# Optimization experiments

Measured on AMD Instinct MI355X. Metric: run time of the kernel, lower is better.

Reference implementation:

```python
import jax, jax.numpy as jnp
import numpy as np

N = 20000      # nodes
E = 400000     # edges
D = 256        # input_dim == hidden_dim
L = 4          # num_layers
EIN = 32       # edgenet_input_dim // 2
EH = 128       # edge parser hidden
NC = 2         # num_classes
JK = L * D     # 1024
BN_EPS = 1e-5


def setup_inputs() -> dict:
    key = jax.random.key(0)
    ks = jax.random.split(key, 16)
    s = 0.05
    inp = {
        "features": jax.random.normal(ks[0], (N, D), jnp.float32),
        "edge_index": jax.random.randint(ks[1], (2, E), 0, N, dtype=jnp.int64),
        "edgenet_input": jax.random.normal(ks[2], (E, 2 * EIN), jnp.float32),
        # ChebConv weights: [layer, k, in, out] (all layers 256->256, K=3, no bias)
        "cheb_w": jax.random.normal(ks[3], (L, 3, D, D), jnp.float32) * s,
        # EdgeEncoder (PAE-style) parser: Linear(32,128)+ReLU+BN+Linear(128,128)
        "en_w1": jax.random.normal(ks[4], (EIN, EH), jnp.float32) * s,
        "en_b1": jnp.zeros((EH,), jnp.float32),
        "en_g1": jnp.ones((EH,), jnp.float32),
        "en_be1": jnp.zeros((EH,), jnp.float32),
        "en_w2": jax.random.normal(ks[5], (EH, EH), jnp.float32) * s,
        "en_b2": jnp.zeros((EH,), jnp.float32),
        # cls head: Linear(1024,256)+ReLU+BN(256)+Linear(256,2)
        "cls_w1": jax.random.normal(ks[6], (JK, 256), jnp.float32) * s,
        "cls_b1": jnp.zeros((256,), jnp.float32),
        "cls_g": jnp.ones((256,), jnp.float32),
        "cls_b": jnp.zeros((256,), jnp.float32),
        "cls_w2": jax.random.normal(ks[7], (256, NC), jnp.float32) * s,
        "cls_b2": jnp.zeros((NC,), jnp.float32),
    }
    return inp


def _bn_eval(x, g, b):
    # eval-mode BatchNorm1d with fresh running stats (mean=0, var=1)
    return x * (g / jnp.sqrt(1.0 + BN_EPS)) + b


def reference(features, edge_index, edgenet_input, cheb_w,
              en_w1, en_b1, en_g1, en_be1, en_w2, en_b2,
              cls_w1, cls_b1, cls_g, cls_b, cls_w2, cls_b2):
    row, col = edge_index[0], edge_index[1]

    # ---- EdgeEncoder (PAE): shared parser on both halves + cosine sim ----
    def parser(x):
        h = jnp.maximum(x @ en_w1 + en_b1, 0.0)
        h = _bn_eval(h, en_g1, en_be1)
        return h @ en_w2 + en_b2

    half = edgenet_input.shape[1] // 2
    h1 = parser(edgenet_input[:, :half])
    h2 = parser(edgenet_input[:, half:])
    n1 = jnp.maximum(jnp.linalg.norm(h1, axis=1), 1e-8)
    n2 = jnp.maximum(jnp.linalg.norm(h2, axis=1), 1e-8)
    cos = jnp.sum(h1 * h2, axis=1) / (n1 * n2)
    edge_weight = (cos + 1.0) * 0.5  # [E]

    # ---- ChebConv sym normalization (lambda_max=2): L_hat = -D^-1/2 A D^-1/2 ----
    deg = jax.ops.segment_sum(edge_weight, row, num_segments=N)
    dis = jnp.where(deg > 0, jax.lax.rsqrt(jnp.maximum(deg, 1e-30)), 0.0)
    norm = -dis[row] * edge_weight * dis[col]  # [E]

    def prop(x):  # out[col] += norm * x[row]
        return jax.ops.segment_sum(x[row] * norm[:, None], col, num_segments=N)

    # ---- stacked ChebConv (K=3, no bias) + ReLU + JK concat ----
    x = features
    jk = None
    for i in range(L):
        W = cheb_w[i]
        Tx0 = x
        Tx1 = prop(Tx0)
        Tx2 = 2.0 * prop(Tx1) - Tx0
        h = jnp.maximum(Tx0 @ W[0] + Tx1 @ W[1] + Tx2 @ W[2], 0.0)
        jk = h if i == 0 else jnp.concatenate([jk, h], axis=1)
        x = h

    # ---- cls head ----
    z = jnp.maximum(jk @ cls_w1 + cls_b1, 0.0)
    z = _bn_eval(z, cls_g, cls_b)
    logit = z @ cls_w2 + cls_b2
    return (logit, edge_weight)
```

## Files before the change

kernel.cpp:

```cpp
#include <hip/hip_runtime.h>
#include <hip/hip_bf16.h>

#define NN 20000
#define EE 400000
#define RSBN 0.9999950000374997f

typedef __attribute__((ext_vector_type(8))) short short8;
typedef __attribute__((ext_vector_type(8))) unsigned short ushort8;
typedef __attribute__((ext_vector_type(4))) float floatx4;

__device__ __forceinline__ short f2bf(float f) {
  union { float f; unsigned u; } v; v.f = f;
  unsigned r = v.u + 0x7fffu + ((v.u >> 16) & 1u);
  return (short)(r >> 16);
}
__device__ __forceinline__ unsigned f2bf2(float x, float y) {
  union { __hip_bfloat162 h; unsigned u; } v;
  v.h = __float22bfloat162_rn(make_float2(x, y));
  return v.u;
}
__device__ __forceinline__ float bf2f(unsigned short u) {
  union { unsigned u; float f; } v; v.u = ((unsigned)u) << 16;
  return v.f;
}
__device__ __forceinline__ void gl_lds16(const void* g, void* l) {
  __builtin_amdgcn_global_load_lds(
      (const __attribute__((address_space(1))) unsigned*)g,
      (__attribute__((address_space(3))) unsigned*)l, 16, 0, 0);
}

__global__ __launch_bounds__(256) void ewconv_kernel(
    const float* __restrict__ w1, const float* __restrict__ w2,
    const float* __restrict__ g1, const float* __restrict__ be1,
    const float* __restrict__ b1, const float* __restrict__ b2,
    unsigned short* __restrict__ ewf)
{
  int tid = threadIdx.x;
#pragma unroll
  for (int i = 0; i < 16; i++) {
    int idx = i * 256 + tid;
    int k = idx >> 7, n = idx & 127;
    int pos = ((n >> 4) * 64 + (k >> 3) * 16 + (n & 15)) * 8 + (k & 7);
    ewf[pos] = f2bf(w1[idx]);
  }
#pragma unroll
  for (int i = 0; i < 64; i++) {
    int idx = i * 256 + tid;
    int k = idx >> 7, n = idx & 127;
    int pos = (((k >> 5) * 8 + (n >> 4)) * 64 + ((k >> 3) & 3) * 16 + (n & 15)) * 8 + (k & 7);
    ewf[4096 + pos] = f2bf(w2[idx] * g1[k] * RSBN);
  }
  float* fb = (float*)(ewf + 20480);
  if (tid < 128) {
    fb[tid] = b1[tid];
    float acc = b2[tid];
    for (int k = 0; k < 128; k++) acc += be1[k] * w2[k * 128 + tid] * g1[k] * RSBN;
    fb[128 + tid] = acc;
  }
}

#define ASP 136
__global__ __launch_bounds__(512, 4) void edge_kernel(
    const float* __restrict__ xin, const int* __restrict__ eidx,
    const unsigned short* __restrict__ ewf,
    float* __restrict__ ew_out,
    float* __restrict__ deg, int* __restrict__ cnt)
{
  __shared__ short wbuf[20992];
  __shared__ short as_s[128 * ASP];

  int tid = threadIdx.x;
  int lane = tid & 63;
  int wv = tid >> 6;
  int l15 = lane & 15;
  int quad = lane >> 4;

#pragma unroll
  for (int i = 0; i < 5; i++)
    gl_lds16(ewf + (i * 512 + tid) * 8, &wbuf[(i * 512 + tid) * 8]);
  if (tid < 64)
    gl_lds16(ewf + (2560 + tid) * 8, &wbuf[(2560 + tid) * 8]);

  const short* w1f = wbuf;
  const short* w2f = wbuf + 4096;

  int rowbase = blockIdx.x * 128 + wv * 16;

  short8 af;
  {
    const float* xp = xin + (size_t)(rowbase + l15) * 32 + quad * 8;
    float4 v0 = *(const float4*)xp;
    float4 v1 = *(const float4*)(xp + 4);
    union { short8 s; unsigned u[4]; } a;
    a.u[0] = f2bf2(v0.x, v0.y); a.u[1] = f2bf2(v0.z, v0.w);
    a.u[2] = f2bf2(v1.x, v1.y); a.u[3] = f2bf2(v1.z, v1.w);
    af = a.s;
  }

  __syncthreads();

  const float* fb = (const float*)(wbuf + 20480);
  float b1j[8], b2j[8];
#pragma unroll
  for (int c = 0; c < 8; c++) {
    b1j[c] = fb[c * 16 + l15];
    b2j[c] = fb[128 + c * 16 + l15];
  }

  floatx4 acc[8];
#pragma unroll
  for (int c = 0; c < 8; c++) {
    floatx4 z = {b1j[c], b1j[c], b1j[c], b1j[c]};
    acc[c] = __builtin_amdgcn_mfma_f32_16x16x32_bf16(
        af, *(const short8*)&w1f[(c * 64 + lane) * 8], z, 0, 0, 0);
  }

#pragma unroll
  for (int c = 0; c < 8; c++)
#pragma unroll
    for (int r = 0; r < 4; r += 2) {
      unsigned pk = f2bf2(fmaxf(acc[c][r], 0.f), fmaxf(acc[c][r + 1], 0.f));
      int base = (wv * 16 + quad * 4 + r) * ASP + c * 16 + l15;
      as_s[base] = (short)(pk & 0xffff);
      as_s[base + ASP] = (short)(pk >> 16);
    }

  floatx4 acc2[8];
#pragma unroll
  for (int c = 0; c < 8; c++) acc2[c] = (floatx4){b2j[c], b2j[c], b2j[c], b2j[c]};
#pragma unroll
  for (int s = 0; s < 4; s++) {
    short8 a2 = *(const short8*)&as_s[(wv * 16 + l15) * ASP + s * 32 + quad * 8];
#pragma unroll
    for (int c = 0; c < 8; c++) {
      short8 bf = *(const short8*)&w2f[((s * 8 + c) * 64 + lane) * 8];
      acc2[c] = __builtin_amdgcn_mfma_f32_16x16x32_bf16(a2, bf, acc2[c], 0, 0, 0);
    }
  }

  float p[2], qq[2], rr[2];
#pragma unroll
  for (int i = 0; i < 2; i++) { p[i] = 0.f; qq[i] = 0.f; rr[i] = 0.f; }
#pragma unroll
  for (int c = 0; c < 8; c++)
#pragma unroll
    for (int i = 0; i < 2; i++) {
      float hx = acc2[c][2 * i];
      float hy = acc2[c][2 * i + 1];
      p[i]  += hx * hy;
      qq[i] += hx * hx;
      rr[i] += hy * hy;
    }
#pragma unroll
  for (int m = 1; m < 16; m <<= 1)
#pragma unroll
    for (int i = 0; i < 2; i++) {
      p[i]  += __shfl_xor(p[i], m, 64);
      qq[i] += __shfl_xor(qq[i], m, 64);
      rr[i] += __shfl_xor(rr[i], m, 64);
    }
  if (l15 == 0) {
#pragma unroll
    for (int i = 0; i < 2; i++) {
      int row = rowbase + quad * 4 + 2 * i;
      int e = row >> 1;
      float n1 = fmaxf(sqrtf(qq[i]), 1e-8f);
      float n2 = fmaxf(sqrtf(rr[i]), 1e-8f);
      float w = (p[i] / (n1 * n2) + 1.f) * 0.5f;
      ew_out[e] = w;
      atomicAdd(deg + eidx[e], w);
      atomicAdd(cnt + eidx[EE + e], 1);
    }
  }
}

__global__ __launch_bounds__(256) void fconv_kernel(const float* __restrict__ src,
                                                    unsigned short* __restrict__ dst) {
  size_t i = ((size_t)blockIdx.x * 256 + threadIdx.x) * 8;
  float4 a = *(const float4*)(src + i);
  float4 b = *(const float4*)(src + i + 4);
  union { ushort8 s; unsigned u[4]; } o;
  o.u[0] = f2bf2(a.x, a.y); o.u[1] = f2bf2(a.z, a.w);
  o.u[2] = f2bf2(b.x, b.y); o.u[3] = f2bf2(b.z, b.w);
  *(ushort8*)(dst + i) = o.s;
}

__global__ __launch_bounds__(256) void wconv_kernel(
    const float* __restrict__ cheb_w, const float* __restrict__ cls_w1,
    unsigned short* __restrict__ wtc, unsigned short* __restrict__ clsT)
{
  __shared__ unsigned short tile[64][80];
  int z = blockIdx.z;
  const float* src; unsigned short* dst; int ldk;
  if (z < 12) {
    int l = z / 3, c = z % 3;
    src = cheb_w + (size_t)z * 65536;
    dst = wtc + (size_t)l * 196608 + c * 256;
    ldk = 768;
  } else {
    int c = z - 12;
    src = cls_w1 + (size_t)c * 65536;
    dst = clsT + c * 256;
    ldk = 1024;
  }
  int t = threadIdx.x;
  int k0 = blockIdx.x * 64, n0 = blockIdx.y * 64;
#pragma unroll
  for (int pass = 0; pass < 4; pass++) {
    int kk = pass * 16 + (t >> 4);
    int nl = (t & 15) * 4;
    float4 v = *(const float4*)(src + (size_t)(k0 + kk) * 256 + n0 + nl);
    tile[nl + 0][kk] = f2bf(v.x);
    tile[nl + 1][kk] = f2bf(v.y);
    tile[nl + 2][kk] = f2bf(v.z);
    tile[nl + 3][kk] = f2bf(v.w);
  }
  __syncthreads();
  int nl = t >> 2, kc = (t & 3) * 16;
  ushort8 v0 = *(const ushort8*)&tile[nl][kc];
  ushort8 v1 = *(const ushort8*)&tile[nl][kc + 8];
  unsigned short* dp = dst + (size_t)(n0 + nl) * ldk + k0 + kc;
  *(ushort8*)dp = v0;
  *(ushort8*)(dp + 8) = v1;
}

__global__ void dis_kernel(const float* __restrict__ deg, float* __restrict__ dis) {
  int i = blockIdx.x * 256 + threadIdx.x;
  if (i < NN) {
    float d = deg[i];
    dis[i] = d > 0.f ? 1.f / sqrtf(fmaxf(d, 1e-30f)) : 0.f;
  }
}

__global__ __launch_bounds__(1024) void scan_kernel(const int* __restrict__ cnt, int* __restrict__ ptr) {
  __shared__ int sums[1024];
  int tid = threadIdx.x;
  const int n = NN;
  const int chunk = (n + 1023) / 1024;
  int base = tid * chunk;
  int s = 0;
  for (int i = 0; i < chunk; i++) {
    int idx = base + i;
    if (idx < n) s += (cnt[idx] + 3) & ~3;
  }
  sums[tid] = s;
  __syncthreads();
  for (int off = 1; off < 1024; off <<= 1) {
    int v = (tid >= off) ? sums[tid - off] : 0;
    __syncthreads();
    sums[tid] += v;
    __syncthreads();
  }
  int run = (tid == 0) ? 0 : sums[tid - 1];
  for (int i = 0; i < chunk; i++) {
    int idx = base + i;
    if (idx < n) { ptr[idx] = run; run += (cnt[idx] + 3) & ~3; }
  }
  if (tid == 1023) ptr[n] = run;
}

__global__ void fill_kernel(const int* __restrict__ eidx, const float* __restrict__ ew,
                            const float* __restrict__ dis, const int* __restrict__ ptr,
                            int* __restrict__ fill, int* __restrict__ cidx, float* __restrict__ cval) {
  int e = blockIdx.x * 256 + threadIdx.x;
  if (e < EE) {
    int r = eidx[e], c = eidx[EE + e];
    float nv = -dis[r] * ew[e] * dis[c];
    int pos = ptr[c] + atomicAdd(&fill[c], 1);
    cidx[pos] = r;
    cval[pos] = nv;
  }
}

__global__ __launch_bounds__(256) void prop_kernel(
    const unsigned short* __restrict__ x, int ldx,
    const int* __restrict__ cidx, const float* __restrict__ cval,
    const int* __restrict__ ptr,
    unsigned short* __restrict__ y, int ldy,
    float alpha, const unsigned short* __restrict__ sub, int ldsub)
{
  int sliceid = blockIdx.x & 7;
  int colslice = sliceid >> 1;
  int chunk = (blockIdx.x >> 3) * 2 + (sliceid & 1);
  int c = chunk * 32 + (threadIdx.x >> 3);
  if (c >= NN) return;
  int d = colslice * 64 + (threadIdx.x & 7) * 8;
  int p0 = ptr[c], p1 = ptr[c + 1];
  float a[8] = {0.f, 0.f, 0.f, 0.f, 0.f, 0.f, 0.f, 0.f};
  if (p0 < p1) {
    int4 r4 = *(const int4*)(cidx + p0);
    float4 w4 = *(const float4*)(cval + p0);
    ushort8 v0 = *(const ushort8*)(x + (size_t)r4.x * ldx + d);
    ushort8 v1 = *(const ushort8*)(x + (size_t)r4.y * ldx + d);
    ushort8 v2 = *(const ushort8*)(x + (size_t)r4.z * ldx + d);
    ushort8 v3 = *(const ushort8*)(x + (size_t)r4.w * ldx + d);
    for (int p = p0 + 4; p < p1; p += 4) {
      int4 r4n = *(const int4*)(cidx + p);
      float4 w4n = *(const float4*)(cval + p);
      ushort8 n0 = *(const ushort8*)(x + (size_t)r4n.x * ldx + d);
      ushort8 n1 = *(const ushort8*)(x + (size_t)r4n.y * ldx + d);
      ushort8 n2 = *(const ushort8*)(x + (size_t)r4n.z * ldx + d);
      ushort8 n3 = *(const ushort8*)(x + (size_t)r4n.w * ldx + d);
#pragma unroll
      for (int j = 0; j < 8; j++)
        a[j] += w4.x * bf2f(v0[j]) + w4.y * bf2f(v1[j]) + w4.z * bf2f(v2[j]) + w4.w * bf2f(v3[j]);
      w4 = w4n; v0 = n0; v1 = n1; v2 = n2; v3 = n3;
    }
#pragma unroll
    for (int j = 0; j < 8; j++)
      a[j] += w4.x * bf2f(v0[j]) + w4.y * bf2f(v1[j]) + w4.z * bf2f(v2[j]) + w4.w * bf2f(v3[j]);
  }
  union { ushort8 s; unsigned u[4]; } o;
  if (sub) {
    ushort8 sv = *(const ushort8*)(sub + (size_t)c * ldsub + d);
#pragma unroll
    for (int j = 0; j < 8; j += 2)
      o.u[j >> 1] = f2bf2(alpha * a[j] - bf2f(sv[j]), alpha * a[j + 1] - bf2f(sv[j + 1]));
  } else {
#pragma unroll
    for (int j = 0; j < 8; j += 2)
      o.u[j >> 1] = f2bf2(a[j], a[j + 1]);
  }
  *(ushort8*)(y + (size_t)c * ldy + d) = o.s;
}

__global__ __launch_bounds__(256, 4) void mgemm_kernel(
    const unsigned short* A0, const unsigned short* A1,
    const unsigned short* A2, const unsigned short* A3,
    int l0, int l1, int l2, int l3, int nchunks,
    const unsigned short* __restrict__ BT, int ldbt,
    unsigned short* __restrict__ Cb, float* __restrict__ Cf, int ldc, int M,
    const float* __restrict__ bias, const float* __restrict__ bng,
    const float* __restrict__ bnb)
{
  __shared__ short As[4 * 64 * 8];
  __shared__ short Bs[4 * 128 * 8];
  int tid = threadIdx.x;
  int lane = tid & 63;
  int wv = tid >> 6;
  int l15 = lane & 15, quad = lane >> 4;
  int wr = wv >> 1, wc = wv & 1;
  int m0 = blockIdx.x * 64, n0 = blockIdx.y * 128;

  const unsigned short* Ap[4] = {A0, A1, A2, A3};
  int Al[4] = {l0, l1, l2, l3};

  int arow = tid & 63, ac = tid >> 6;
  int brow = tid & 127, bc = tid >> 7;

  floatx4 acc[2][4];
#pragma unroll
  for (int mi = 0; mi < 2; mi++)
#pragma unroll
    for (int nj = 0; nj < 4; nj++) acc[mi][nj] = (floatx4){0.f, 0.f, 0.f, 0.f};

  for (int c = 0; c < nchunks; c++) {
    const unsigned short* Abase = Ap[c] + (size_t)(m0 + arow) * Al[c] + ac * 8;
    const unsigned short* Bbase = BT + (size_t)(n0 + brow) * ldbt + c * 256 + bc * 8;
#pragma unroll 1
    for (int kb = 0; kb < 256; kb += 32) {
      __syncthreads();
      gl_lds16(Abase + kb, &As[tid * 8]);
      gl_lds16(Bbase + kb, &Bs[tid * 8]);
      gl_lds16(Bbase + 16 + kb, &Bs[(tid + 256) * 8]);
      __syncthreads();
      short8 af[2], bfv[4];
#pragma unroll
      for (int mi = 0; mi < 2; mi++)
        af[mi] = *(const short8*)&As[(quad * 64 + wr * 32 + mi * 16 + l15) * 8];
#pragma unroll
      for (int nj = 0; nj < 4; nj++)
        bfv[nj] = *(const short8*)&Bs[(quad * 128 + wc * 64 + nj * 16 + l15) * 8];
#pragma unroll
      for (int nj = 0; nj < 4; nj++)
#pragma unroll
        for (int mi = 0; mi < 2; mi++)
          acc[mi][nj] = __builtin_amdgcn_mfma_f32_16x16x32_bf16(af[mi], bfv[nj], acc[mi][nj], 0, 0, 0);
    }
  }

  if (Cb) {
#pragma unroll
    for (int mi = 0; mi < 2; mi++)
#pragma unroll
      for (int r = 0; r < 4; r++) {
        int row = m0 + wr * 32 + mi * 16 + quad * 4 + r;
        if (row < M) {
#pragma unroll
          for (int nj = 0; nj < 4; nj++) {
            int col = n0 + wc * 64 + nj * 16 + l15;
            Cb[(size_t)row * ldc + col] = (unsigned short)f2bf(fmaxf(acc[mi][nj][r], 0.f));
          }
        }
      }
  } else {
    float bs[4], g[4], bb[4];
#pragma unroll
    for (int nj = 0; nj < 4; nj++) {
      int col = n0 + wc * 64 + nj * 16 + l15;
      bs[nj] = bias[col]; g[nj] = bng[col] * RSBN; bb[nj] = bnb[col];
    }
#pragma unroll
    for (int mi = 0; mi < 2; mi++)
#pragma unroll
      for (int r = 0; r < 4; r++) {
        int row = m0 + wr * 32 + mi * 16 + quad * 4 + r;
        if (row < M) {
#pragma unroll
          for (int nj = 0; nj < 4; nj++) {
            int col = n0 + wc * 64 + nj * 16 + l15;
            float v = fmaxf(acc[mi][nj][r] + bs[nj], 0.f) * g[nj] + bb[nj];
            Cf[(size_t)row * ldc + col] = v;
          }
        }
      }
  }
}

__global__ __launch_bounds__(256) void logit_kernel(
    const float* __restrict__ z, const float* __restrict__ w2,
    const float* __restrict__ b2, float* __restrict__ out)
{
  int node = blockIdx.x * 4 + (threadIdx.x >> 6);
  if (node >= NN) return;
  int lane = threadIdx.x & 63;
  int k = lane * 4;
  float4 zv = *(const float4*)(z + (size_t)node * 256 + k);
  float4 wa = *(const float4*)(w2 + k * 2);
  float4 wb = *(const float4*)(w2 + k * 2 + 4);
  float a0 = zv.x * wa.x + zv.y * wa.z + zv.z * wb.x + zv.w * wb.z;
  float a1 = zv.x * wa.y + zv.y * wa.w + zv.z * wb.y + zv.w * wb.w;
#pragma unroll
  for (int m = 32; m >= 1; m >>= 1) {
    a0 += __shfl_xor(a0, m, 64);
    a1 += __shfl_xor(a1, m, 64);
  }
  if (lane == 0) {
    out[(size_t)node * 2]     = a0 + b2[0];
    out[(size_t)node * 2 + 1] = a1 + b2[1];
  }
}

extern "C" void kernel_launch(void* const* d_in, const int* in_sizes, int n_in,
                              void* d_out, int out_size, void* d_ws, size_t ws_size,
                              hipStream_t stream) {
  const float* features = (const float*)d_in[0];
  const int*   eidx     = (const int*)d_in[1];
  const float* xin      = (const float*)d_in[2];
  const float* cheb_w   = (const float*)d_in[3];
  const float* en_w1    = (const float*)d_in[4];
  const float* en_b1    = (const float*)d_in[5];
  const float* en_g1    = (const float*)d_in[6];
  const float* en_be1   = (const float*)d_in[7];
  const float* en_w2    = (const float*)d_in[8];
  const float* en_b2    = (const float*)d_in[9];
  const float* cls_w1   = (const float*)d_in[10];
  const float* cls_b1   = (const float*)d_in[11];
  const float* cls_g    = (const float*)d_in[12];
  const float* cls_b    = (const float*)d_in[13];
  const float* cls_w2   = (const float*)d_in[14];
  const float* cls_b2   = (const float*)d_in[15];
  float* out = (float*)d_out;

  char* ws = (char*)d_ws;
  size_t off = 0;
  auto alloc = [&](size_t bytes) -> void* {
    void* p = ws + off;
    off += (bytes + 255) & ~(size_t)255;
    return p;
  };
  const int CSRN = EE + 4 * NN;
  float* deg  = (float*)alloc((size_t)NN * 4);
  int*   cnt  = (int*)  alloc((size_t)NN * 4);
  int*   fil  = (int*)  alloc((size_t)NN * 4);
  float* cval = (float*)alloc((size_t)CSRN * 4);
  int*   cidx = (int*)  alloc((size_t)CSRN * 4);
  size_t zero_len = off;
  float* dis  = (float*)alloc((size_t)NN * 4);
  int*   ptr  = (int*)  alloc((size_t)(NN + 1) * 4);
  unsigned short* featb = (unsigned short*)alloc((size_t)NN * 256 * 2);
  unsigned short* Tx1   = (unsigned short*)alloc((size_t)NN * 256 * 2);
  unsigned short* Tx2   = (unsigned short*)alloc((size_t)NN * 256 * 2);
  unsigned short* jk    = (unsigned short*)alloc((size_t)NN * 1024 * 2);
  float* zbuf = (float*)alloc((size_t)NN * 256 * 4);
  unsigned short* wtc   = (unsigned short*)alloc((size_t)4 * 196608 * 2);
  unsigned short* clsT  = (unsigned short*)alloc((size_t)256 * 1024 * 2);
  unsigned short* ewf   = (unsigned short*)alloc((size_t)20992 * 2);
  alloc(262144);

  float* ew = out + (size_t)NN * 2;

  hipMemsetAsync(deg, 0, zero_len, stream);

  ewconv_kernel<<<1, 256, 0, stream>>>(en_w1, en_w2, en_g1, en_be1, en_b1, en_b2, ewf);
  edge_kernel<<<6250, 512, 0, stream>>>(xin, eidx, ewf, ew, deg, cnt);
  fconv_kernel<<<2500, 256, 0, stream>>>(features, featb);
  wconv_kernel<<<dim3(4, 4, 16), 256, 0, stream>>>(cheb_w, cls_w1, wtc, clsT);
  dis_kernel<<<(NN + 255) / 256, 256, 0, stream>>>(deg, dis);
  scan_kernel<<<1, 1024, 0, stream>>>(cnt, ptr);
  fill_kernel<<<(EE + 255) / 256, 256, 0, stream>>>(eidx, ew, dis, ptr, fil, cidx, cval);

  dim3 ggrid(313, 2);
  for (int i = 0; i < 4; i++) {
    const unsigned short* x = (i == 0) ? featb : (jk + (size_t)(i - 1) * 256);
    int ldx = (i == 0) ? 256 : 1024;
    prop_kernel<<<2504, 256, 0, stream>>>(x, ldx, cidx, cval, ptr, Tx1, 256, 1.f, nullptr, 0);
    prop_kernel<<<2504, 256, 0, stream>>>(Tx1, 256, cidx, cval, ptr, Tx2, 256, 2.f, x, ldx);
    mgemm_kernel<<<ggrid, 256, 0, stream>>>(x, Tx1, Tx2, nullptr, ldx, 256, 256, 0, 3,
                                            wtc + (size_t)i * 196608, 768,
                                            jk + (size_t)i * 256, nullptr, 1024, NN,
                                            nullptr, nullptr, nullptr);
  }

  mgemm_kernel<<<ggrid, 256, 0, stream>>>(jk, jk + 256, jk + 512, jk + 768,
                                          1024, 1024, 1024, 1024, 4, clsT, 1024,
                                          nullptr, zbuf, 256, NN,
                                          cls_b1, cls_g, cls_b);
  logit_kernel<<<NN / 4, 256, 0, stream>>>(zbuf, cls_w2, cls_b2, out);
}
```

Baseline: 646.8 us.

## Keep edge MLP hidden activations in registers and fold dis into fill

The edge encoder now computes the first layer transposed, so the ReLU output already sits in the B-operand layout of a 16x16x16 bf16 MFMA for the second layer. This removes the shared-memory staging buffer and its round trip. The W2 prepack layout and the cosine reduction shuffles are changed to match, and launch bounds rise to 6 blocks per CU. Separately, the dis kernel is removed and fill_kernel computes rsqrt(deg) inline, trading one launch for redundant per-edge rsqrt work.

```diff
diff --git a/kernel.cpp b/kernel.cpp
--- a/kernel.cpp
+++ b/kernel.cpp
@@ -7,6 +7,7 @@
 
 typedef __attribute__((ext_vector_type(8))) short short8;
 typedef __attribute__((ext_vector_type(8))) unsigned short ushort8;
+typedef __attribute__((ext_vector_type(4))) short bf4;
 typedef __attribute__((ext_vector_type(4))) float floatx4;
 
 __device__ __forceinline__ short f2bf(float f) {
@@ -27,6 +28,17 @@
   __builtin_amdgcn_global_load_lds(
       (const __attribute__((address_space(1))) unsigned*)g,
       (__attribute__((address_space(3))) unsigned*)l, 16, 0, 0);
+}
+
+__device__ __forceinline__ floatx4 mfma16(bf4 a, bf4 b, floatx4 c) {
+#if __has_builtin(__builtin_amdgcn_mfma_f32_16x16x16bf16_1k)
+  return __builtin_amdgcn_mfma_f32_16x16x16bf16_1k(a, b, c, 0, 0, 0);
+#else
+  floatx4 d;
+  asm volatile("v_mfma_f32_16x16x16_bf16 %0, %1, %2, %3"
+               : "=&v"(d) : "v"(a), "v"(b), "v"(c));
+  return d;
+#endif
 }
 
 __global__ __launch_bounds__(256) void ewconv_kernel(
@@ -47,7 +59,9 @@
   for (int i = 0; i < 64; i++) {
     int idx = i * 256 + tid;
     int k = idx >> 7, n = idx & 127;
-    int pos = (((k >> 5) * 8 + (n >> 4)) * 64 + ((k >> 3) & 3) * 16 + (n & 15)) * 8 + (k & 7);
+    int u = k >> 4, q = (k >> 2) & 3, j = k & 3;
+    int t = n >> 4, l = n & 15;
+    int pos = (((u * 8 + t) * 4 + q) * 16 + l) * 4 + j;
     ewf[4096 + pos] = f2bf(w2[idx] * g1[k] * RSBN);
   }
   float* fb = (float*)(ewf + 20480);
@@ -59,15 +73,13 @@
   }
 }
 
-#define ASP 136
-__global__ __launch_bounds__(512, 4) void edge_kernel(
+__global__ __launch_bounds__(512, 6) void edge_kernel(
     const float* __restrict__ xin, const int* __restrict__ eidx,
     const unsigned short* __restrict__ ewf,
     float* __restrict__ ew_out,
     float* __restrict__ deg, int* __restrict__ cnt)
 {
   __shared__ short wbuf[20992];
-  __shared__ short as_s[128 * ASP];
 
   int tid = threadIdx.x;
   int lane = tid & 63;
@@ -100,77 +112,60 @@
   __syncthreads();
 
   const float* fb = (const float*)(wbuf + 20480);
-  float b1j[8], b2j[8];
-#pragma unroll
-  for (int c = 0; c < 8; c++) {
-    b1j[c] = fb[c * 16 + l15];
-    b2j[c] = fb[128 + c * 16 + l15];
-  }
-
-  floatx4 acc[8];
-#pragma unroll
-  for (int c = 0; c < 8; c++) {
-    floatx4 z = {b1j[c], b1j[c], b1j[c], b1j[c]};
-    acc[c] = __builtin_amdgcn_mfma_f32_16x16x32_bf16(
-        af, *(const short8*)&w1f[(c * 64 + lane) * 8], z, 0, 0, 0);
-  }
-
-#pragma unroll
-  for (int c = 0; c < 8; c++)
-#pragma unroll
-    for (int r = 0; r < 4; r += 2) {
-      unsigned pk = f2bf2(fmaxf(acc[c][r], 0.f), fmaxf(acc[c][r + 1], 0.f));
-      int base = (wv * 16 + quad * 4 + r) * ASP + c * 16 + l15;
-      as_s[base] = (short)(pk & 0xffff);
-      as_s[base + ASP] = (short)(pk >> 16);
+
+  floatx4 acc1[8];
+#pragma unroll
+  for (int t = 0; t < 8; t++) {
+    floatx4 z = *(const floatx4*)&fb[t * 16 + quad * 4];
+    acc1[t] = __builtin_amdgcn_mfma_f32_16x16x32_bf16(
+        *(const short8*)&w1f[(t * 64 + lane) * 8], af, z, 0, 0, 0);
+  }
+
+  bf4 pb[8];
+#pragma unroll
+  for (int u = 0; u < 8; u++) {
+    union { bf4 s; unsigned w[2]; } o;
+    o.w[0] = f2bf2(fmaxf(acc1[u][0], 0.f), fmaxf(acc1[u][1], 0.f));
+    o.w[1] = f2bf2(fmaxf(acc1[u][2], 0.f), fmaxf(acc1[u][3], 0.f));
+    pb[u] = o.s;
+  }
+
+  floatx4 acc2[8];
+#pragma unroll
+  for (int t = 0; t < 8; t++)
+    acc2[t] = *(const floatx4*)&fb[128 + t * 16 + quad * 4];
+#pragma unroll
+  for (int u = 0; u < 8; u++)
+#pragma unroll
+    for (int t = 0; t < 8; t++) {
+      bf4 a4 = *(const bf4*)&w2f[((u * 8 + t) * 64 + lane) * 4];
+      acc2[t] = mfma16(a4, pb[u], acc2[t]);
     }
 
-  floatx4 acc2[8];
-#pragma unroll
-  for (int c = 0; c < 8; c++) acc2[c] = (floatx4){b2j[c], b2j[c], b2j[c], b2j[c]};
-#pragma unroll
-  for (int s = 0; s < 4; s++) {
-    short8 a2 = *(const short8*)&as_s[(wv * 16 + l15) * ASP + s * 32 + quad * 8];
-#pragma unroll
-    for (int c = 0; c < 8; c++) {
-      short8 bf = *(const short8*)&w2f[((s * 8 + c) * 64 + lane) * 8];
-      acc2[c] = __builtin_amdgcn_mfma_f32_16x16x32_bf16(a2, bf, acc2[c], 0, 0, 0);
+  float qq = 0.f, pp = 0.f;
+#pragma unroll
+  for (int t = 0; t < 8; t++)
+#pragma unroll
+    for (int r = 0; r < 4; r++) {
+      float h = acc2[t][r];
+      float hp = __shfl_xor(h, 1, 64);
+      qq += h * h;
+      pp += h * hp;
     }
-  }
-
-  float p[2], qq[2], rr[2];
-#pragma unroll
-  for (int i = 0; i < 2; i++) { p[i] = 0.f; qq[i] = 0.f; rr[i] = 0.f; }
-#pragma unroll
-  for (int c = 0; c < 8; c++)
-#pragma unroll
-    for (int i = 0; i < 2; i++) {
-      float hx = acc2[c][2 * i];
-      float hy = acc2[c][2 * i + 1];
-      p[i]  += hx * hy;
-      qq[i] += hx * hx;
-      rr[i] += hy * hy;
-    }
-#pragma unroll
-  for (int m = 1; m < 16; m <<= 1)
-#pragma unroll
-    for (int i = 0; i < 2; i++) {
-      p[i]  += __shfl_xor(p[i], m, 64);
-      qq[i] += __shfl_xor(qq[i], m, 64);
-      rr[i] += __shfl_xor(rr[i], m, 64);
-    }
-  if (l15 == 0) {
-#pragma unroll
-    for (int i = 0; i < 2; i++) {
-      int row = rowbase + quad * 4 + 2 * i;
-      int e = row >> 1;
-      float n1 = fmaxf(sqrtf(qq[i]), 1e-8f);
-      float n2 = fmaxf(sqrtf(rr[i]), 1e-8f);
-      float w = (p[i] / (n1 * n2) + 1.f) * 0.5f;
-      ew_out[e] = w;
-      atomicAdd(deg + eidx[e], w);
-      atomicAdd(cnt + eidx[EE + e], 1);
-    }
+  qq += __shfl_xor(qq, 16, 64);
+  pp += __shfl_xor(pp, 16, 64);
+  qq += __shfl_xor(qq, 32, 64);
+  pp += __shfl_xor(pp, 32, 64);
+  float rr = __shfl_xor(qq, 1, 64);
+
+  if (quad == 0 && !(l15 & 1)) {
+    int e = (rowbase + l15) >> 1;
+    float n1 = fmaxf(sqrtf(qq), 1e-8f);
+    float n2 = fmaxf(sqrtf(rr), 1e-8f);
+    float w = (pp / (n1 * n2) + 1.f) * 0.5f;
+    ew_out[e] = w;
+    atomicAdd(deg + eidx[e], w);
+    atomicAdd(cnt + eidx[EE + e], 1);
   }
 }
 
@@ -224,14 +219,6 @@
   *(ushort8*)(dp + 8) = v1;
 }
 
-__global__ void dis_kernel(const float* __restrict__ deg, float* __restrict__ dis) {
-  int i = blockIdx.x * 256 + threadIdx.x;
-  if (i < NN) {
-    float d = deg[i];
-    dis[i] = d > 0.f ? 1.f / sqrtf(fmaxf(d, 1e-30f)) : 0.f;
-  }
-}
-
 __global__ __launch_bounds__(1024) void scan_kernel(const int* __restrict__ cnt, int* __restrict__ ptr) {
   __shared__ int sums[1024];
   int tid = threadIdx.x;
@@ -260,12 +247,15 @@
 }
 
 __global__ void fill_kernel(const int* __restrict__ eidx, const float* __restrict__ ew,
-                            const float* __restrict__ dis, const int* __restrict__ ptr,
+                            const float* __restrict__ deg, const int* __restrict__ ptr,
                             int* __restrict__ fill, int* __restrict__ cidx, float* __restrict__ cval) {
   int e = blockIdx.x * 256 + threadIdx.x;
   if (e < EE) {
     int r = eidx[e], c = eidx[EE + e];
-    float nv = -dis[r] * ew[e] * dis[c];
+    float dr = deg[r], dc = deg[c];
+    float ir = dr > 0.f ? 1.f / sqrtf(fmaxf(dr, 1e-30f)) : 0.f;
+    float ic = dc > 0.f ? 1.f / sqrtf(fmaxf(dc, 1e-30f)) : 0.f;
+    float nv = -ir * ew[e] * ic;
     int pos = ptr[c] + atomicAdd(&fill[c], 1);
     cidx[pos] = r;
     cval[pos] = nv;
@@ -476,7 +466,6 @@
   float* cval = (float*)alloc((size_t)CSRN * 4);
   int*   cidx = (int*)  alloc((size_t)CSRN * 4);
   size_t zero_len = off;
-  float* dis  = (float*)alloc((size_t)NN * 4);
   int*   ptr  = (int*)  alloc((size_t)(NN + 1) * 4);
   unsigned short* featb = (unsigned short*)alloc((size_t)NN * 256 * 2);
   unsigned short* Tx1   = (unsigned short*)alloc((size_t)NN * 256 * 2);
@@ -496,9 +485,8 @@
   edge_kernel<<<6250, 512, 0, stream>>>(xin, eidx, ewf, ew, deg, cnt);
   fconv_kernel<<<2500, 256, 0, stream>>>(features, featb);
   wconv_kernel<<<dim3(4, 4, 16), 256, 0, stream>>>(cheb_w, cls_w1, wtc, clsT);
-  dis_kernel<<<(NN + 255) / 256, 256, 0, stream>>>(deg, dis);
   scan_kernel<<<1, 1024, 0, stream>>>(cnt, ptr);
-  fill_kernel<<<(EE + 255) / 256, 256, 0, stream>>>(eidx, ew, dis, ptr, fil, cidx, cval);
+  fill_kernel<<<(EE + 255) / 256, 256, 0, stream>>>(eidx, ew, deg, ptr, fil, cidx, cval);
 
   dim3 ggrid(313, 2);
   for (int i = 0; i < 4; i++) {
```

Measured after the change: 646.1 us. No clear change (-0.1%).
